# Kernel optimization log

Measured on AMD Instinct MI355X. Metric: run time of the kernel, lower is better.

## Reference

```python
import jax, jax.numpy as jnp
import numpy as np

N = 50000
E = 640000
D = 128
R = 8
LAMDA = 1


def _conv(x, row, col, edge_type, coef, W, b):
    # Transform every node by every relation weight: [N, R, D]
    xW = jnp.einsum('nd,rdo->nro', x, W)
    # Gather the per-edge transformed source feature: [E, D]
    msg = xW[row, edge_type] * coef[:, None]
    # Scatter-add to target nodes, then bias
    return jax.ops.segment_sum(msg, col, num_segments=N) + b


def setup_inputs() -> dict:
    key = jax.random.key(0)
    ks = jax.random.split(key, 8)
    x = jax.random.normal(ks[0], (N, D), dtype=jnp.float32)
    edge_index = jax.random.randint(ks[1], (2, E), 0, N, dtype=jnp.int64)
    edge_type = jax.random.randint(ks[2], (E,), 0, R, dtype=jnp.int64)
    edge_weight = jax.random.uniform(ks[3], (E,), dtype=jnp.float32)
    # kaiming_uniform_(a=sqrt(5)) on [R, D, D]: bound = sqrt(6/((1+5)*fan_in)) = 1/sqrt(fan_in)
    bound = 1.0 / np.sqrt(D)
    W1 = jax.random.uniform(ks[4], (R, D, D), minval=-bound, maxval=bound, dtype=jnp.float32)
    W2 = jax.random.uniform(ks[5], (R, D, D), minval=-bound, maxval=bound, dtype=jnp.float32)
    b1 = jnp.zeros((D,), dtype=jnp.float32)
    b2 = jnp.zeros((D,), dtype=jnp.float32)
    return {"x": x, "edge_index": edge_index, "edge_type": edge_type,
            "edge_weight": edge_weight, "W1": W1, "b1": b1, "W2": W2, "b2": b2}


def reference(x, edge_index, edge_type, edge_weight, W1, b1, W2, b2):
    row = edge_index[0]  # source nodes (x_j)
    col = edge_index[1]  # target nodes (aggregation)
    deg = jax.ops.segment_sum(jnp.ones((E,), dtype=x.dtype), col, num_segments=N)
    deg_inv_sqrt = jnp.where(deg == 0, 1.0, deg ** -0.5)
    norm = deg_inv_sqrt[row] * deg_inv_sqrt[col]
    coef = norm * edge_weight  # [E]

    z1 = jax.nn.leaky_relu(_conv(x, row, col, edge_type, coef, W1, b1), negative_slope=0.01)
    # dropout is identity in eval mode
    z2 = _conv(z1, row, col, edge_type, coef, W2, b2)

    z_star = (x + z1 + z2) / 4.0
    # z_sharp = sum(temp[LAMDA:]) / (4 - LAMDA) with temp = [x, z1, z2]
    temp = [x, z1, z2]
    z_sharp = temp[LAMDA]
    for i in range(LAMDA + 1, 3):
        z_sharp = z_sharp + temp[i]
    z_sharp = z_sharp / (4.0 - LAMDA)
    return (z_star, z_sharp)
```

## Files before the change

kernel.cpp:

```cpp
#include <hip/hip_runtime.h>
#include <hip/hip_bf16.h>

#define DD 128
#define NREL 8
#define LDHB 1032

typedef float f32x4 __attribute__((ext_vector_type(4)));
typedef short short8 __attribute__((ext_vector_type(8)));

__device__ __forceinline__ float dis_f(float deg) {
    return deg == 0.0f ? 1.0f : rsqrtf(deg);
}

__global__ __launch_bounds__(256) void count_kernel(const int* __restrict__ ei,
                                                    int* __restrict__ cnt, int E) {
    int e = blockIdx.x * blockDim.x + threadIdx.x;
    if (e < E) atomicAdd(&cnt[ei[E + e]], 1);
}

__global__ __launch_bounds__(1024) void scan_kernel(const int* __restrict__ cnt,
                                                    int* __restrict__ cur, int N) {
    __shared__ int s[1024];
    const int t = threadIdx.x;
    const int chunk = (N + 1023) / 1024;
    const int beg = t * chunk, end = min(N, beg + chunk);
    int sum = 0;
    for (int c = beg; c < end; ++c) sum += cnt[c];
    s[t] = sum;
    __syncthreads();
    for (int off = 1; off < 1024; off <<= 1) {
        int add = (t >= off) ? s[t - off] : 0;
        __syncthreads();
        s[t] += add;
        __syncthreads();
    }
    int run = s[t] - sum;
    for (int c = beg; c < end; ++c) { cur[c] = run; run += cnt[c]; }
}

__global__ __launch_bounds__(256) void bucket_kernel(const int* __restrict__ ei,
                                                     const int* __restrict__ et,
                                                     const float* __restrict__ ew,
                                                     const int* __restrict__ cnt,
                                                     int* __restrict__ cur,
                                                     uint2* __restrict__ ebuf, int E) {
    int e = blockIdx.x * blockDim.x + threadIdx.x;
    if (e >= E) return;
    const int row = ei[e], col = ei[E + e];
    const float coef = dis_f((float)cnt[row]) * dis_f((float)cnt[col]) * ew[e];
    const int pos = atomicAdd(&cur[col], 1);
    ebuf[pos] = make_uint2(((unsigned)et[e] << 16) | (unsigned)row, __float_as_uint(coef));
}

__global__ __launch_bounds__(256) void wtrans_kernel(const float* __restrict__ W1,
                                                     const float* __restrict__ W2,
                                                     __hip_bfloat16* __restrict__ BT1,
                                                     __hip_bfloat16* __restrict__ BT2) {
    const int r = blockIdx.x;
    const float* W = blockIdx.y ? W2 : W1;
    __hip_bfloat16* BT = blockIdx.y ? BT2 : BT1;
    const int d = threadIdx.x & 127;
    const int og0 = threadIdx.x >> 7;
    for (int j = 0; j < 64; ++j) {
        const int o = og0 * 64 + j;
        BT[(size_t)o * 1024 + r * DD + d] =
            __float2bfloat16(W[((size_t)r * DD + d) * DD + o]);
    }
}

__global__ __launch_bounds__(256) void xcvt_kernel(const float* __restrict__ x,
                                                   __hip_bfloat16* __restrict__ xb, int total4) {
    int i = blockIdx.x * blockDim.x + threadIdx.x;
    if (i >= total4) return;
    const float4 a = ((const float4*)x)[i];
    __hip_bfloat162 p0 = __float22bfloat162_rn(make_float2(a.x, a.y));
    __hip_bfloat162 p1 = __float22bfloat162_rn(make_float2(a.z, a.w));
    uint2 u;
    u.x = *(unsigned int*)&p0;
    u.y = *(unsigned int*)&p1;
    *(uint2*)&xb[(size_t)i * 4] = u;
}

#define ACCUM(RQ, VV) do {                                              \
    const float cf_ = __uint_as_float((RQ).y);                          \
    const float xl_ = __uint_as_float((VV) << 16);                      \
    const float xh_ = __uint_as_float((VV) & 0xffff0000u);              \
    switch ((RQ).x >> 16) {                                             \
        case 0: acc[0]  += cf_*xl_; acc[1]  += cf_*xh_; break;          \
        case 1: acc[2]  += cf_*xl_; acc[3]  += cf_*xh_; break;          \
        case 2: acc[4]  += cf_*xl_; acc[5]  += cf_*xh_; break;          \
        case 3: acc[6]  += cf_*xl_; acc[7]  += cf_*xh_; break;          \
        case 4: acc[8]  += cf_*xl_; acc[9]  += cf_*xh_; break;          \
        case 5: acc[10] += cf_*xl_; acc[11] += cf_*xh_; break;          \
        case 6: acc[12] += cf_*xl_; acc[13] += cf_*xh_; break;          \
        default: acc[14] += cf_*xl_; acc[15] += cf_*xh_; break;         \
    } } while (0)

template<int LAYER>
__global__ __launch_bounds__(256) void fused_kernel(const __hip_bfloat16* __restrict__ srcb,
                                                    const uint2* __restrict__ ebuf,
                                                    const int* __restrict__ cur,
                                                    const __hip_bfloat16* __restrict__ BT,
                                                    const float* __restrict__ bias,
                                                    const float* __restrict__ x,
                                                    __hip_bfloat16* __restrict__ z1b,
                                                    float* __restrict__ out, int N) {
    __shared__ __hip_bfloat16 hb[16][LDHB];
    const int tid = threadIdx.x;
    const int w = tid >> 6, l = tid & 63;
    const int c0 = blockIdx.x * 16;

    for (int q = 0; q < 4; ++q) {
        const int m = w * 4 + q;
        const int c = c0 + m;
        float acc[16];
        #pragma unroll
        for (int i = 0; i < 16; ++i) acc[i] = 0.f;
        if (c < N) {
            int beg = (c > 0) ? cur[c - 1] : 0;
            int end = cur[c];
            beg = __builtin_amdgcn_readfirstlane(beg);
            end = __builtin_amdgcn_readfirstlane(end);
            int e = beg;
            uint2 qa0 = make_uint2(0u, 0u), qa1 = qa0, qa2 = qa0, qa3 = qa0;
            if (e + 4 <= end) {
                qa0 = ebuf[e]; qa1 = ebuf[e + 1]; qa2 = ebuf[e + 2]; qa3 = ebuf[e + 3];
            }
            while (e + 4 <= end) {
                const unsigned v0 = *(const unsigned*)&srcb[(size_t)(qa0.x & 0xffffu) * DD + 2 * l];
                const unsigned v1 = *(const unsigned*)&srcb[(size_t)(qa1.x & 0xffffu) * DD + 2 * l];
                const unsigned v2 = *(const unsigned*)&srcb[(size_t)(qa2.x & 0xffffu) * DD + 2 * l];
                const unsigned v3 = *(const unsigned*)&srcb[(size_t)(qa3.x & 0xffffu) * DD + 2 * l];
                uint2 qb0, qb1, qb2, qb3;
                const bool more = (e + 8 <= end);
                if (more) {
                    qb0 = ebuf[e + 4]; qb1 = ebuf[e + 5]; qb2 = ebuf[e + 6]; qb3 = ebuf[e + 7];
                }
                ACCUM(qa0, v0); ACCUM(qa1, v1); ACCUM(qa2, v2); ACCUM(qa3, v3);
                if (more) { qa0 = qb0; qa1 = qb1; qa2 = qb2; qa3 = qb3; }
                e += 4;
            }
            for (; e < end; ++e) {
                const uint2 qq = ebuf[e];
                const unsigned vv = *(const unsigned*)&srcb[(size_t)(qq.x & 0xffffu) * DD + 2 * l];
                ACCUM(qq, vv);
            }
        }
        #pragma unroll
        for (int r = 0; r < NREL; ++r) {
            __hip_bfloat162 p = __float22bfloat162_rn(make_float2(acc[2 * r], acc[2 * r + 1]));
            *(unsigned int*)&hb[m][r * DD + 2 * l] = *(unsigned int*)&p;
        }
    }
    __syncthreads();

    const int lk = (l >> 4) * 8;
    const int lr = l & 15;
    f32x4 acc0 = {0.f, 0.f, 0.f, 0.f}, acc1 = {0.f, 0.f, 0.f, 0.f};
    const __hip_bfloat16* bt0 = BT + (size_t)(w * 32 + lr) * 1024 + lk;
    const __hip_bfloat16* bt1 = bt0 + (size_t)16 * 1024;
    const __hip_bfloat16* ha = &hb[lr][lk];
    #pragma unroll 8
    for (int k0 = 0; k0 < 1024; k0 += 32) {
        const short8 a  = *(const short8*)(ha + k0);
        const short8 b0 = *(const short8*)(bt0 + k0);
        const short8 b1 = *(const short8*)(bt1 + k0);
        acc0 = __builtin_amdgcn_mfma_f32_16x16x32_bf16(a, b0, acc0, 0, 0, 0);
        acc1 = __builtin_amdgcn_mfma_f32_16x16x32_bf16(a, b1, acc1, 0, 0, 0);
    }

    const int rbase = (l >> 4) * 4;
    #pragma unroll
    for (int f = 0; f < 2; ++f) {
        const f32x4 av = f ? acc1 : acc0;
        const int o = w * 32 + f * 16 + lr;
        const float bv = bias[o];
        #pragma unroll
        for (int q = 0; q < 4; ++q) {
            const int c = c0 + rbase + q;
            if (c >= N) continue;
            const size_t idx = (size_t)c * DD + o;
            float v = av[q] + bv;
            if (LAYER == 1) {
                v = v >= 0.f ? v : 0.01f * v;
                z1b[idx] = __float2bfloat16(v);
            } else {
                const float z1v = __bfloat162float(z1b[idx]);
                const float xv2 = x[idx];
                out[idx] = (xv2 + z1v + v) * 0.25f;
                out[(size_t)N * DD + idx] = (z1v + v) * (1.f / 3.f);
            }
        }
    }
}

extern "C" void kernel_launch(void* const* d_in, const int* in_sizes, int n_in,
                              void* d_out, int out_size, void* d_ws, size_t ws_size,
                              hipStream_t stream) {
    const float* x  = (const float*)d_in[0];
    const int*   ei = (const int*)d_in[1];
    const int*   et = (const int*)d_in[2];
    const float* ew = (const float*)d_in[3];
    const float* W1 = (const float*)d_in[4];
    const float* b1 = (const float*)d_in[5];
    const float* W2 = (const float*)d_in[6];
    const float* b2 = (const float*)d_in[7];

    const int N = in_sizes[0] / DD;
    const int E = in_sizes[3];
    float* out = (float*)d_out;

    char* w = (char*)d_ws;
    int* cnt = (int*)w;                 w += (size_t)N * 4;
    int* cur = (int*)w;                 w += (size_t)N * 4;
    __hip_bfloat16* BT1 = (__hip_bfloat16*)w;  w += (size_t)DD * NREL * DD * 2;
    __hip_bfloat16* BT2 = (__hip_bfloat16*)w;  w += (size_t)DD * NREL * DD * 2;
    uint2* ebuf = (uint2*)w;            w += (size_t)E * 8;
    __hip_bfloat16* xb = (__hip_bfloat16*)w;   w += (size_t)N * DD * 2;
    __hip_bfloat16* z1b = (__hip_bfloat16*)w;

    hipMemsetAsync(cnt, 0, (size_t)N * 4, stream);

    const int eb = (E + 255) / 256;
    count_kernel<<<eb, 256, 0, stream>>>(ei, cnt, E);
    wtrans_kernel<<<dim3(NREL, 2), 256, 0, stream>>>(W1, W2, BT1, BT2);
    const int t4 = N * DD / 4;
    xcvt_kernel<<<(t4 + 255) / 256, 256, 0, stream>>>(x, xb, t4);
    scan_kernel<<<1, 1024, 0, stream>>>(cnt, cur, N);
    bucket_kernel<<<eb, 256, 0, stream>>>(ei, et, ew, cnt, cur, ebuf, E);

    const int nb = (N + 15) / 16;
    fused_kernel<1><<<nb, 256, 0, stream>>>(xb,  ebuf, cur, BT1, b1, x, z1b, out, N);
    fused_kernel<2><<<nb, 256, 0, stream>>>(z1b, ebuf, cur, BT2, b2, x, z1b, out, N);
}
```

Before: 422.4 us.

## Stage edge records in LDS, widen fused block to 32 nodes, restructure weight transpose

The fused aggregation+GEMM kernel now processes 32 target nodes per 512-thread block. Each block cooperatively loads its contiguous slice of edge records into LDS, and waves read them with readfirstlane broadcasts, gathering 8 neighbour rows at a time. The MFMA stage now shares each B fragment across two 16-row A tiles. The weight-transpose kernel goes through a shared-memory tile so both its loads and stores coalesce, and the scan vectorises its count reads. The aim is to cut scalar global loads of edge records and raise memory-level parallelism. In exchange the block uses more LDS and registers (a 4x16 accumulator per thread), which may limit occupancy.

```diff
diff --git a/kernel.cpp b/kernel.cpp
--- a/kernel.cpp
+++ b/kernel.cpp
@@ -4,6 +4,8 @@
 #define DD 128
 #define NREL 8
 #define LDHB 1032
+#define BC 32
+#define RECCAP 1024
 
 typedef float f32x4 __attribute__((ext_vector_type(4)));
 typedef short short8 __attribute__((ext_vector_type(8)));
@@ -22,10 +24,15 @@
                                                     int* __restrict__ cur, int N) {
     __shared__ int s[1024];
     const int t = threadIdx.x;
-    const int chunk = (N + 1023) / 1024;
+    const int chunk = (((N + 1023) / 1024) + 3) & ~3;
     const int beg = t * chunk, end = min(N, beg + chunk);
     int sum = 0;
-    for (int c = beg; c < end; ++c) sum += cnt[c];
+    int c = beg;
+    for (; c + 4 <= end; c += 4) {
+        const int4 v = *(const int4*)&cnt[c];
+        sum += v.x + v.y + v.z + v.w;
+    }
+    for (; c < end; ++c) sum += cnt[c];
     s[t] = sum;
     __syncthreads();
     for (int off = 1; off < 1024; off <<= 1) {
@@ -35,7 +42,7 @@
         __syncthreads();
     }
     int run = s[t] - sum;
-    for (int c = beg; c < end; ++c) { cur[c] = run; run += cnt[c]; }
+    for (int cc = beg; cc < end; ++cc) { cur[cc] = run; run += cnt[cc]; }
 }
 
 __global__ __launch_bounds__(256) void bucket_kernel(const int* __restrict__ ei,
@@ -56,16 +63,18 @@
                                                      const float* __restrict__ W2,
                                                      __hip_bfloat16* __restrict__ BT1,
                                                      __hip_bfloat16* __restrict__ BT2) {
-    const int r = blockIdx.x;
-    const float* W = blockIdx.y ? W2 : W1;
-    __hip_bfloat16* BT = blockIdx.y ? BT2 : BT1;
+    __shared__ __hip_bfloat16 tile[128][130];
+    const int r = blockIdx.x & 7;
+    const float* W = (blockIdx.x >> 3) ? W2 : W1;
+    __hip_bfloat16* BT = (blockIdx.x >> 3) ? BT2 : BT1;
+    const int o = threadIdx.x & 127;
+    const int h = threadIdx.x >> 7;
+    for (int d = h; d < DD; d += 2)
+        tile[d][o] = __float2bfloat16(W[((size_t)r * DD + d) * DD + o]);
+    __syncthreads();
     const int d = threadIdx.x & 127;
-    const int og0 = threadIdx.x >> 7;
-    for (int j = 0; j < 64; ++j) {
-        const int o = og0 * 64 + j;
-        BT[(size_t)o * 1024 + r * DD + d] =
-            __float2bfloat16(W[((size_t)r * DD + d) * DD + o]);
-    }
+    for (int o2 = h; o2 < DD; o2 += 2)
+        BT[(size_t)o2 * 1024 + r * DD + d] = tile[d][o2];
 }
 
 __global__ __launch_bounds__(256) void xcvt_kernel(const float* __restrict__ x,
@@ -81,74 +90,89 @@
     *(uint2*)&xb[(size_t)i * 4] = u;
 }
 
-#define ACCUM(RQ, VV) do {                                              \
-    const float cf_ = __uint_as_float((RQ).y);                          \
-    const float xl_ = __uint_as_float((VV) << 16);                      \
-    const float xh_ = __uint_as_float((VV) & 0xffff0000u);              \
-    switch ((RQ).x >> 16) {                                             \
-        case 0: acc[0]  += cf_*xl_; acc[1]  += cf_*xh_; break;          \
-        case 1: acc[2]  += cf_*xl_; acc[3]  += cf_*xh_; break;          \
-        case 2: acc[4]  += cf_*xl_; acc[5]  += cf_*xh_; break;          \
-        case 3: acc[6]  += cf_*xl_; acc[7]  += cf_*xh_; break;          \
-        case 4: acc[8]  += cf_*xl_; acc[9]  += cf_*xh_; break;          \
-        case 5: acc[10] += cf_*xl_; acc[11] += cf_*xh_; break;          \
-        case 6: acc[12] += cf_*xl_; acc[13] += cf_*xh_; break;          \
-        default: acc[14] += cf_*xl_; acc[15] += cf_*xh_; break;         \
+#define ACCUM(Q, MS, CF, VV) do {                                          \
+    const float xl_ = __uint_as_float((VV) << 16);                         \
+    const float xh_ = __uint_as_float((VV) & 0xffff0000u);                 \
+    switch ((MS) >> 16) {                                                  \
+        case 0: acc[Q][0]  += (CF)*xl_; acc[Q][1]  += (CF)*xh_; break;     \
+        case 1: acc[Q][2]  += (CF)*xl_; acc[Q][3]  += (CF)*xh_; break;     \
+        case 2: acc[Q][4]  += (CF)*xl_; acc[Q][5]  += (CF)*xh_; break;     \
+        case 3: acc[Q][6]  += (CF)*xl_; acc[Q][7]  += (CF)*xh_; break;     \
+        case 4: acc[Q][8]  += (CF)*xl_; acc[Q][9]  += (CF)*xh_; break;     \
+        case 5: acc[Q][10] += (CF)*xl_; acc[Q][11] += (CF)*xh_; break;     \
+        case 6: acc[Q][12] += (CF)*xl_; acc[Q][13] += (CF)*xh_; break;     \
+        default: acc[Q][14] += (CF)*xl_; acc[Q][15] += (CF)*xh_; break;    \
     } } while (0)
 
 template<int LAYER>
-__global__ __launch_bounds__(256) void fused_kernel(const __hip_bfloat16* __restrict__ srcb,
-                                                    const uint2* __restrict__ ebuf,
-                                                    const int* __restrict__ cur,
-                                                    const __hip_bfloat16* __restrict__ BT,
-                                                    const float* __restrict__ bias,
-                                                    const float* __restrict__ x,
-                                                    __hip_bfloat16* __restrict__ z1b,
-                                                    float* __restrict__ out, int N) {
-    __shared__ __hip_bfloat16 hb[16][LDHB];
+__global__ __launch_bounds__(512, 4) void fused_kernel(const __hip_bfloat16* __restrict__ srcb,
+                                                       const uint2* __restrict__ ebuf,
+                                                       const int* __restrict__ cur,
+                                                       const __hip_bfloat16* __restrict__ BT,
+                                                       const float* __restrict__ bias,
+                                                       const float* __restrict__ x,
+                                                       __hip_bfloat16* __restrict__ z1b,
+                                                       float* __restrict__ out, int N) {
+    __shared__ __hip_bfloat16 hb[BC][LDHB];
+    __shared__ uint2 recs[RECCAP];
     const int tid = threadIdx.x;
     const int w = tid >> 6, l = tid & 63;
-    const int c0 = blockIdx.x * 16;
-
+    const int c0 = blockIdx.x * BC;
+
+    float acc[4][16];
+    #pragma unroll
+    for (int q = 0; q < 4; ++q)
+        #pragma unroll
+        for (int i = 0; i < 16; ++i) acc[q][i] = 0.f;
+
+    const int B0 = (c0 > 0) ? cur[c0 - 1] : 0;
+    const int B1 = cur[min(c0 + BC - 1, N - 1)];
+
+    for (int cb = B0; cb < B1; cb += RECCAP) {
+        const int ce = min(B1, cb + RECCAP);
+        for (int i = cb + tid; i < ce; i += 512) recs[i - cb] = ebuf[i];
+        __syncthreads();
+        #pragma unroll
+        for (int q = 0; q < 4; ++q) {
+            const int c = c0 + w * 4 + q;
+            if (c < N) {
+                const int bc = (c > 0) ? cur[c - 1] : 0;
+                const int ec = cur[c];
+                const int lo = max(bc, cb), hi = min(ec, ce);
+                int e = lo;
+                while (e + 8 <= hi) {
+                    unsigned ms[8]; float cf[8]; unsigned v[8];
+                    #pragma unroll
+                    for (int i = 0; i < 8; ++i) {
+                        const uint2 rr = recs[e - cb + i];
+                        ms[i] = (unsigned)__builtin_amdgcn_readfirstlane((int)rr.x);
+                        cf[i] = __uint_as_float((unsigned)__builtin_amdgcn_readfirstlane((int)rr.y));
+                    }
+                    #pragma unroll
+                    for (int i = 0; i < 8; ++i)
+                        v[i] = *(const unsigned*)&srcb[(size_t)(ms[i] & 0xffffu) * DD + 2 * l];
+                    #pragma unroll
+                    for (int i = 0; i < 8; ++i) ACCUM(q, ms[i], cf[i], v[i]);
+                    e += 8;
+                }
+                for (; e < hi; ++e) {
+                    const uint2 rr = recs[e - cb];
+                    const unsigned m1 = (unsigned)__builtin_amdgcn_readfirstlane((int)rr.x);
+                    const float c1 = __uint_as_float((unsigned)__builtin_amdgcn_readfirstlane((int)rr.y));
+                    const unsigned v1 = *(const unsigned*)&srcb[(size_t)(m1 & 0xffffu) * DD + 2 * l];
+                    ACCUM(q, m1, c1, v1);
+                }
+            }
+        }
+        __syncthreads();
+    }
+
+    #pragma unroll
     for (int q = 0; q < 4; ++q) {
         const int m = w * 4 + q;
-        const int c = c0 + m;
-        float acc[16];
-        #pragma unroll
-        for (int i = 0; i < 16; ++i) acc[i] = 0.f;
-        if (c < N) {
-            int beg = (c > 0) ? cur[c - 1] : 0;
-            int end = cur[c];
-            beg = __builtin_amdgcn_readfirstlane(beg);
-            end = __builtin_amdgcn_readfirstlane(end);
-            int e = beg;
-            uint2 qa0 = make_uint2(0u, 0u), qa1 = qa0, qa2 = qa0, qa3 = qa0;
-            if (e + 4 <= end) {
-                qa0 = ebuf[e]; qa1 = ebuf[e + 1]; qa2 = ebuf[e + 2]; qa3 = ebuf[e + 3];
-            }
-            while (e + 4 <= end) {
-                const unsigned v0 = *(const unsigned*)&srcb[(size_t)(qa0.x & 0xffffu) * DD + 2 * l];
-                const unsigned v1 = *(const unsigned*)&srcb[(size_t)(qa1.x & 0xffffu) * DD + 2 * l];
-                const unsigned v2 = *(const unsigned*)&srcb[(size_t)(qa2.x & 0xffffu) * DD + 2 * l];
-                const unsigned v3 = *(const unsigned*)&srcb[(size_t)(qa3.x & 0xffffu) * DD + 2 * l];
-                uint2 qb0, qb1, qb2, qb3;
-                const bool more = (e + 8 <= end);
-                if (more) {
-                    qb0 = ebuf[e + 4]; qb1 = ebuf[e + 5]; qb2 = ebuf[e + 6]; qb3 = ebuf[e + 7];
-                }
-                ACCUM(qa0, v0); ACCUM(qa1, v1); ACCUM(qa2, v2); ACCUM(qa3, v3);
-                if (more) { qa0 = qb0; qa1 = qb1; qa2 = qb2; qa3 = qb3; }
-                e += 4;
-            }
-            for (; e < end; ++e) {
-                const uint2 qq = ebuf[e];
-                const unsigned vv = *(const unsigned*)&srcb[(size_t)(qq.x & 0xffffu) * DD + 2 * l];
-                ACCUM(qq, vv);
-            }
-        }
         #pragma unroll
         for (int r = 0; r < NREL; ++r) {
-            __hip_bfloat162 p = __float22bfloat162_rn(make_float2(acc[2 * r], acc[2 * r + 1]));
+            __hip_bfloat162 p = __float22bfloat162_rn(make_float2(acc[q][2 * r], acc[q][2 * r + 1]));
             *(unsigned int*)&hb[m][r * DD + 2 * l] = *(unsigned int*)&p;
         }
     }
@@ -157,27 +181,27 @@
     const int lk = (l >> 4) * 8;
     const int lr = l & 15;
     f32x4 acc0 = {0.f, 0.f, 0.f, 0.f}, acc1 = {0.f, 0.f, 0.f, 0.f};
-    const __hip_bfloat16* bt0 = BT + (size_t)(w * 32 + lr) * 1024 + lk;
-    const __hip_bfloat16* bt1 = bt0 + (size_t)16 * 1024;
-    const __hip_bfloat16* ha = &hb[lr][lk];
+    const __hip_bfloat16* bt = BT + (size_t)(w * 16 + lr) * 1024 + lk;
+    const __hip_bfloat16* h0 = &hb[lr][lk];
+    const __hip_bfloat16* h1 = &hb[16 + lr][lk];
     #pragma unroll 8
     for (int k0 = 0; k0 < 1024; k0 += 32) {
-        const short8 a  = *(const short8*)(ha + k0);
-        const short8 b0 = *(const short8*)(bt0 + k0);
-        const short8 b1 = *(const short8*)(bt1 + k0);
-        acc0 = __builtin_amdgcn_mfma_f32_16x16x32_bf16(a, b0, acc0, 0, 0, 0);
-        acc1 = __builtin_amdgcn_mfma_f32_16x16x32_bf16(a, b1, acc1, 0, 0, 0);
+        const short8 b  = *(const short8*)(bt + k0);
+        const short8 a0 = *(const short8*)(h0 + k0);
+        const short8 a1 = *(const short8*)(h1 + k0);
+        acc0 = __builtin_amdgcn_mfma_f32_16x16x32_bf16(a0, b, acc0, 0, 0, 0);
+        acc1 = __builtin_amdgcn_mfma_f32_16x16x32_bf16(a1, b, acc1, 0, 0, 0);
     }
 
     const int rbase = (l >> 4) * 4;
+    const int o = w * 16 + lr;
+    const float bv = bias[o];
     #pragma unroll
-    for (int f = 0; f < 2; ++f) {
-        const f32x4 av = f ? acc1 : acc0;
-        const int o = w * 32 + f * 16 + lr;
-        const float bv = bias[o];
+    for (int t = 0; t < 2; ++t) {
+        const f32x4 av = t ? acc1 : acc0;
         #pragma unroll
         for (int q = 0; q < 4; ++q) {
-            const int c = c0 + rbase + q;
+            const int c = c0 + t * 16 + rbase + q;
             if (c >= N) continue;
             const size_t idx = (size_t)c * DD + o;
             float v = av[q] + bv;
@@ -223,13 +247,13 @@
 
     const int eb = (E + 255) / 256;
     count_kernel<<<eb, 256, 0, stream>>>(ei, cnt, E);
-    wtrans_kernel<<<dim3(NREL, 2), 256, 0, stream>>>(W1, W2, BT1, BT2);
+    wtrans_kernel<<<16, 256, 0, stream>>>(W1, W2, BT1, BT2);
     const int t4 = N * DD / 4;
     xcvt_kernel<<<(t4 + 255) / 256, 256, 0, stream>>>(x, xb, t4);
     scan_kernel<<<1, 1024, 0, stream>>>(cnt, cur, N);
     bucket_kernel<<<eb, 256, 0, stream>>>(ei, et, ew, cnt, cur, ebuf, E);
 
-    const int nb = (N + 15) / 16;
-    fused_kernel<1><<<nb, 256, 0, stream>>>(xb,  ebuf, cur, BT1, b1, x, z1b, out, N);
-    fused_kernel<2><<<nb, 256, 0, stream>>>(z1b, ebuf, cur, BT2, b2, x, z1b, out, N);
-}
+    const int nb = (N + BC - 1) / BC;
+    fused_kernel<1><<<nb, 512, 0, stream>>>(xb,  ebuf, cur, BT1, b1, x, z1b, out, N);
+    fused_kernel<2><<<nb, 512, 0, stream>>>(z1b, ebuf, cur, BT2, b2, x, z1b, out, N);
+}
```

Measured after the change: 407.8 us. 3.4% less time.
